# Optimization experiments

Measured on AMD Instinct MI355X. Metric: run time of the kernel, lower is better.

The kernel has to match this reference:

```python
import jax, jax.numpy as jnp
import numpy as np

C = 256
NUM_HEADS = 8
GROUPS = C // 8
EPS = 1e-5


def conv1x1(x, w, b=None):
    # x: (B,C,H,W), w: (O,C)
    y = jnp.einsum('bchw,oc->bohw', x, w)
    if b is not None:
        y = y + b[None, :, None, None]
    return y


def dwconv3x3_s2(x, w):
    # depthwise 3x3, stride 2, padding 1; w: (C,1,3,3)
    return jax.lax.conv_general_dilated(
        x, w, window_strides=(2, 2), padding=((1, 1), (1, 1)),
        feature_group_count=x.shape[1],
        dimension_numbers=('NCHW', 'OIHW', 'NCHW'))


def group_norm(x, scale, bias, groups=GROUPS, eps=EPS):
    B, Cc, H, W = x.shape
    xg = x.reshape(B, groups, Cc // groups, H, W)
    mu = xg.mean(axis=(2, 3, 4), keepdims=True)
    var = xg.var(axis=(2, 3, 4), keepdims=True)
    xn = (xg - mu) * jax.lax.rsqrt(var + eps)
    return xn.reshape(B, Cc, H, W) * scale[None, :, None, None] + bias[None, :, None, None]


def silu(x):
    return x * jax.nn.sigmoid(x)


def downsample_branch(x, dw, gn1_s, gn1_b, pw, gn2_s, gn2_b):
    y = dwconv3x3_s2(x, dw)
    y = silu(group_norm(y, gn1_s, gn1_b))
    y = conv1x1(y, pw)
    y = silu(group_norm(y, gn2_s, gn2_b))
    return y


def setup_inputs() -> dict:
    key = jax.random.key(0)
    ks = jax.random.split(key, 20)
    s = 1.0 / np.sqrt(C)
    inp = {
        'x': jax.random.normal(ks[0], (32, C, 32, 32), dtype=jnp.float32),
        'wq': jax.random.normal(ks[1], (C, C), dtype=jnp.float32) * s,
        'bq': jnp.zeros((C,), jnp.float32),
        'wk': jax.random.normal(ks[2], (C, C), dtype=jnp.float32) * s,
        'bk': jnp.zeros((C,), jnp.float32),
        'wv': jax.random.normal(ks[3], (C, C), dtype=jnp.float32) * s,
        'bv': jnp.zeros((C,), jnp.float32),
        'k_dw': jax.random.normal(ks[4], (C, 1, 3, 3), dtype=jnp.float32) * (1.0 / 3.0),
        'k_gn1_s': jnp.ones((C,), jnp.float32), 'k_gn1_b': jnp.zeros((C,), jnp.float32),
        'k_pw': jax.random.normal(ks[5], (C, C), dtype=jnp.float32) * s,
        'k_gn2_s': jnp.ones((C,), jnp.float32), 'k_gn2_b': jnp.zeros((C,), jnp.float32),
        'v_dw': jax.random.normal(ks[6], (C, 1, 3, 3), dtype=jnp.float32) * (1.0 / 3.0),
        'v_gn1_s': jnp.ones((C,), jnp.float32), 'v_gn1_b': jnp.zeros((C,), jnp.float32),
        'v_pw': jax.random.normal(ks[7], (C, C), dtype=jnp.float32) * s,
        'v_gn2_s': jnp.ones((C,), jnp.float32), 'v_gn2_b': jnp.zeros((C,), jnp.float32),
    }
    return inp


def reference(x, wq, bq, wk, bk, wv, bv,
              k_dw, k_gn1_s, k_gn1_b, k_pw, k_gn2_s, k_gn2_b,
              v_dw, v_gn1_s, v_gn1_b, v_pw, v_gn2_s, v_gn2_b):
    B, Cc, H, W = x.shape
    nh = NUM_HEADS
    Dh = Cc // nh
    q = conv1x1(x, wq, bq)
    k = conv1x1(x, wk, bk)
    v = conv1x1(x, wv, bv)
    k = downsample_branch(k, k_dw, k_gn1_s, k_gn1_b, k_pw, k_gn2_s, k_gn2_b)
    v = downsample_branch(v, v_dw, v_gn1_s, v_gn1_b, v_pw, v_gn2_s, v_gn2_b)
    # view (B, nh, Dh, N) then transpose to (B, nh, N, Dh)
    qh = q.reshape(B, nh, Dh, -1).transpose(0, 1, 3, 2)
    kh = k.reshape(B, nh, Dh, -1).transpose(0, 1, 3, 2)
    vh = v.reshape(B, nh, Dh, -1).transpose(0, 1, 3, 2)
    scores = jnp.einsum('bhnd,bhmd->bhnm', qh, kh) / jnp.sqrt(jnp.float32(Dh))
    attn = jax.nn.softmax(scores, axis=-1)
    out = jnp.einsum('bhnm,bhmd->bhnd', attn, vh)  # (B,nh,N,Dh)
    out = out.transpose(0, 1, 3, 2).reshape(B, Cc, H, W)
    return out
```

## Files before the change

kernel.cpp:

```cpp
#include <hip/hip_runtime.h>
#include <cstddef>

#define B_  32
#define C_  256
#define N_  1024
#define M_  256
#define NH_ 8
#define DH_ 32

typedef __attribute__((ext_vector_type(4))) float f32x4;
typedef _Float16 half8h __attribute__((ext_vector_type(8)));
typedef _Float16 half4h __attribute__((ext_vector_type(4)));
typedef _Float16 half2h __attribute__((ext_vector_type(2)));

#define GLD16(g, l) __builtin_amdgcn_global_load_lds( \
    (const __attribute__((address_space(1))) unsigned int*)(g), \
    (__attribute__((address_space(3))) unsigned int*)(l), 16, 0, 0)

__global__ __launch_bounds__(256) void prep(
    const float* __restrict__ x,
    const float* __restrict__ w0, const float* __restrict__ w1,
    const float* __restrict__ w2, const float* __restrict__ w3,
    const float* __restrict__ w4,
    _Float16* __restrict__ xt, _Float16* __restrict__ wf5)
{
    const int bx = blockIdx.x;
    const int tid = threadIdx.x;

    if (bx < 2048) {
        __shared__ float tile[64][65];
        const int k0 = (bx & 3) * 64;
        const int n0 = ((bx >> 2) & 15) * 64;
        const int b  = bx >> 6;
        #pragma unroll
        for (int i = 0; i < 4; ++i) {
            const int kl = (tid >> 4) + i * 16;
            float4 v = *(const float4*)&x[((size_t)(b * C_) + k0 + kl) * N_ + n0 + (tid & 15) * 4];
            tile[(tid & 15) * 4 + 0][kl] = v.x;
            tile[(tid & 15) * 4 + 1][kl] = v.y;
            tile[(tid & 15) * 4 + 2][kl] = v.z;
            tile[(tid & 15) * 4 + 3][kl] = v.w;
        }
        __syncthreads();
        #pragma unroll
        for (int i = 0; i < 4; ++i) {
            const int nl = (tid >> 4) + i * 16;
            const int kl = (tid & 15) * 4;
            half4h hv;
            hv[0] = (_Float16)tile[nl][kl + 0];
            hv[1] = (_Float16)tile[nl][kl + 1];
            hv[2] = (_Float16)tile[nl][kl + 2];
            hv[3] = (_Float16)tile[nl][kl + 3];
            *(half4h*)&xt[((size_t)(b * N_) + n0 + nl) * C_ + k0 + kl] = hv;
        }
    } else {
        const int wb = bx - 2048;
        const int which = wb >> 4;
        const int off0  = (wb & 15) * 4096;
        const float* src = which == 0 ? w0 : which == 1 ? w1 : which == 2 ? w2
                          : which == 3 ? w3 : w4;
        _Float16* dst = wf5 + (size_t)which * 65536 + off0;
        #pragma unroll
        for (int j = 0; j < 16; ++j)
            dst[tid + j * 256] = (_Float16)src[off0 + tid + j * 256];
    }
}

__global__ __launch_bounds__(256) void qkv_gemm(
    const _Float16* __restrict__ wf5, const _Float16* __restrict__ XT,
    const float* __restrict__ bq, const float* __restrict__ bk,
    const float* __restrict__ bv,
    _Float16* __restrict__ yq, _Float16* __restrict__ yk,
    _Float16* __restrict__ yv)
{
    __shared__ _Float16 Ah[128][32];
    __shared__ _Float16 Bh[128][32];

    const int z = blockIdx.z;
    const int which = z >> 5;
    const int b = z & 31;
    const _Float16* Wf = wf5 + (size_t)which * 65536;
    const float* bias = which == 0 ? bq : which == 1 ? bk : bv;
    _Float16* Y = which == 0 ? yq : which == 1 ? yk : yv;

    const int row0 = blockIdx.x * 128;
    const int n0   = blockIdx.y * 128;
    const int tid  = threadIdx.x;
    const int lane = tid & 63, w = tid >> 6;
    const int wm = (w >> 1) * 64, wn = (w & 1) * 64;
    const int l16 = lane & 15, lq = lane >> 4;

    const _Float16* XTb = XT + ((size_t)(b * N_) + n0) * C_;

    const int sr = lane >> 2;
    const int sc = (lane & 3) * 8;
    const _Float16* Ag0 = Wf  + (size_t)(row0 + w * 32 + sr) * C_ + sc;
    const _Float16* Ag1 = Ag0 + (size_t)16 * C_;
    const _Float16* Bg0 = XTb + (size_t)(w * 32 + sr) * C_ + sc;
    const _Float16* Bg1 = Bg0 + (size_t)16 * C_;
    _Float16* ldsA0 = &Ah[w * 32][0];
    _Float16* ldsA1 = &Ah[w * 32 + 16][0];
    _Float16* ldsB0 = &Bh[w * 32][0];
    _Float16* ldsB1 = &Bh[w * 32 + 16][0];

    f32x4 acc[4][4];
    #pragma unroll
    for (int i = 0; i < 4; ++i)
        #pragma unroll
        for (int j = 0; j < 4; ++j)
            #pragma unroll
            for (int r = 0; r < 4; ++r) acc[i][j][r] = 0.f;

    for (int k0 = 0; k0 < C_; k0 += 32) {
        __syncthreads();
        GLD16(Ag0 + k0, ldsA0);
        GLD16(Ag1 + k0, ldsA1);
        GLD16(Bg0 + k0, ldsB0);
        GLD16(Bg1 + k0, ldsB1);
        __syncthreads();

        half8h af[4], bf[4];
        #pragma unroll
        for (int t = 0; t < 4; ++t) {
            af[t] = *(const half8h*)&Ah[wm + t * 16 + l16][lq * 8];
            bf[t] = *(const half8h*)&Bh[wn + t * 16 + l16][lq * 8];
        }
        #pragma unroll
        for (int mt = 0; mt < 4; ++mt)
            #pragma unroll
            for (int nt = 0; nt < 4; ++nt)
                acc[mt][nt] = __builtin_amdgcn_mfma_f32_16x16x32_f16(af[mt], bf[nt], acc[mt][nt], 0, 0, 0);
    }

    #pragma unroll
    for (int mt = 0; mt < 4; ++mt) {
        #pragma unroll
        for (int r = 0; r < 4; ++r) {
            const int row = row0 + wm + mt * 16 + lq * 4 + r;
            const float bv_ = bias[row];
            #pragma unroll
            for (int nt = 0; nt < 4; ++nt)
                Y[((size_t)(b * C_) + row) * N_ + n0 + wn + nt * 16 + l16] =
                    (_Float16)(acc[mt][nt][r] + bv_);
        }
    }
}

__global__ __launch_bounds__(256) void dw_gn(
    const _Float16* __restrict__ kin, const _Float16* __restrict__ vin,
    const float* __restrict__ kdw, const float* __restrict__ vdw,
    const float* __restrict__ kg1s, const float* __restrict__ kg1b,
    const float* __restrict__ vg1s, const float* __restrict__ vg1b,
    _Float16* __restrict__ kdT, _Float16* __restrict__ vdT)
{
    __shared__ _Float16 Xs[8192];
    __shared__ float red[8];
    const int bx = blockIdx.x;
    const int branch = bx >> 10;
    const int b = (bx >> 5) & 31;
    const int g = bx & 31;
    const _Float16* in = branch ? vin : kin;
    const float* dw = branch ? vdw : kdw;
    const float* gs = branch ? vg1s : kg1s;
    const float* gb = branch ? vg1b : kg1b;
    _Float16* outT = branch ? vdT : kdT;

    const int tid = threadIdx.x;

    {
        const _Float16* src = in + ((size_t)(b * C_) + g * 8) * 1024;
        #pragma unroll
        for (int i = 0; i < 4; ++i)
            *(half8h*)&Xs[tid * 8 + i * 2048] =
                *(const half8h*)&src[tid * 8 + i * 2048];
    }
    __syncthreads();

    const int oy = tid >> 4, ox = tid & 15;
    const int iy0 = oy*2 - 1, ix0 = ox*2 - 1;

    float vals[8];
    float s1 = 0.f, s2 = 0.f;
    #pragma unroll
    for (int cc = 0; cc < 8; ++cc) {
        const int c = g*8 + cc;
        const _Float16* ip = &Xs[cc * 1024];
        const float* wp = dw + c*9;
        float s = 0.f;
        #pragma unroll
        for (int dy = 0; dy < 3; ++dy) {
            const int iy = iy0 + dy;
            if (iy < 0 || iy > 31) continue;
            #pragma unroll
            for (int dx = 0; dx < 3; ++dx) {
                const int ix = ix0 + dx;
                if (ix < 0 || ix > 31) continue;
                s += (float)ip[iy*32 + ix] * wp[dy*3 + dx];
            }
        }
        vals[cc] = s;
        s1 += s; s2 += s*s;
    }
    #pragma unroll
    for (int off = 32; off > 0; off >>= 1) {
        s1 += __shfl_down(s1, off);
        s2 += __shfl_down(s2, off);
    }
    const int lane = tid & 63, wid = tid >> 6;
    if (lane == 0) { red[wid] = s1; red[4 + wid] = s2; }
    __syncthreads();
    s1 = red[0] + red[1] + red[2] + red[3];
    s2 = red[4] + red[5] + red[6] + red[7];
    const float mean = s1 * (1.f/2048.f);
    const float var  = s2 * (1.f/2048.f) - mean*mean;
    const float rstd = rsqrtf(var + 1e-5f);

    half8h o;
    #pragma unroll
    for (int cc = 0; cc < 8; ++cc) {
        const int c = g*8 + cc;
        const float xn = (vals[cc] - mean) * rstd * gs[c] + gb[c];
        o[cc] = (_Float16)(xn / (1.f + __expf(-xn)));
    }
    *(half8h*)&outT[((size_t)(b * M_) + tid) * C_ + g * 8] = o;
}

__global__ __launch_bounds__(256) void pw_gn2(
    const _Float16* __restrict__ wf5,
    const _Float16* __restrict__ kdT, const _Float16* __restrict__ vdT,
    const float* __restrict__ kg2s, const float* __restrict__ kg2b,
    const float* __restrict__ vg2s, const float* __restrict__ vg2b,
    _Float16* __restrict__ k2, _Float16* __restrict__ v2)
{
    __shared__ _Float16 Wlds[32][264];
    __shared__ _Float16 Bs[256][32];
    __shared__ float gmean[4], grstd[4];

    const int ch0 = blockIdx.x * 32;
    const int b   = blockIdx.y;
    const int branch = blockIdx.z;
    const _Float16* Wsrc = wf5 + (size_t)(3 + branch) * 65536;
    const _Float16* inT = branch ? vdT : kdT;
    const float* gs = branch ? vg2s : kg2s;
    const float* gb = branch ? vg2b : kg2b;
    _Float16* outp = branch ? v2 : k2;

    const int tid = threadIdx.x;
    const int lane = tid & 63, w = tid >> 6;
    const int l16 = lane & 15, quad = lane >> 4;

    {
        const int row = tid >> 3;
        const int off = (tid & 7) * 32;
        #pragma unroll
        for (int j = 0; j < 4; ++j)
            *(int4*)&Wlds[row][off + j * 8] =
                *(const int4*)&Wsrc[(size_t)(ch0 + row) * C_ + off + j * 8];
    }

    f32x4 acc[2][4];
    #pragma unroll
    for (int i = 0; i < 2; ++i)
        #pragma unroll
        for (int j = 0; j < 4; ++j)
            #pragma unroll
            for (int r = 0; r < 4; ++r) acc[i][j][r] = 0.f;

    const _Float16* inb = inT + (size_t)(b * M_) * C_;
    const int sr = lane >> 2;
    const int sc = (lane & 3) * 8;
    const _Float16* Bg = inb + (size_t)(w * 64 + sr) * C_ + sc;

    for (int k0 = 0; k0 < C_; k0 += 32) {
        __syncthreads();
        GLD16(Bg + k0,             &Bs[w * 64][0]);
        GLD16(Bg + 16 * C_ + k0,   &Bs[w * 64 + 16][0]);
        GLD16(Bg + 32 * C_ + k0,   &Bs[w * 64 + 32][0]);
        GLD16(Bg + 48 * C_ + k0,   &Bs[w * 64 + 48][0]);
        __syncthreads();

        half8h af[2], bf[4];
        #pragma unroll
        for (int mt = 0; mt < 2; ++mt)
            af[mt] = *(const half8h*)&Wlds[mt * 16 + l16][k0 + quad * 8];
        #pragma unroll
        for (int nt = 0; nt < 4; ++nt)
            bf[nt] = *(const half8h*)&Bs[w * 64 + nt * 16 + l16][quad * 8];
        #pragma unroll
        for (int mt = 0; mt < 2; ++mt)
            #pragma unroll
            for (int nt = 0; nt < 4; ++nt)
                acc[mt][nt] = __builtin_amdgcn_mfma_f32_16x16x32_f16(af[mt], bf[nt], acc[mt][nt], 0, 0, 0);
    }

    __syncthreads();
    _Float16 (*Rs)[264] = Wlds;
    #pragma unroll
    for (int mt = 0; mt < 2; ++mt)
        #pragma unroll
        for (int nt = 0; nt < 4; ++nt)
            #pragma unroll
            for (int r = 0; r < 4; ++r)
                Rs[mt * 16 + quad * 4 + r][w * 64 + nt * 16 + l16] = (_Float16)acc[mt][nt][r];
    __syncthreads();

    {
        float s1 = 0.f, s2 = 0.f;
        #pragma unroll
        for (int r = 0; r < 8; ++r)
            #pragma unroll
            for (int j = 0; j < 4; ++j) {
                const float vv = (float)Rs[w * 8 + r][lane * 4 + j];
                s1 += vv; s2 += vv * vv;
            }
        #pragma unroll
        for (int off = 32; off > 0; off >>= 1) {
            s1 += __shfl_xor(s1, off);
            s2 += __shfl_xor(s2, off);
        }
        if (lane == 0) {
            const float mean = s1 * (1.f / 2048.f);
            const float var  = s2 * (1.f / 2048.f) - mean * mean;
            gmean[w] = mean;
            grstd[w] = rsqrtf(var + 1e-5f);
        }
    }
    __syncthreads();

    #pragma unroll
    for (int cc = 0; cc < 32; ++cc) {
        const int g = cc >> 3;
        const float xn = ((float)Rs[cc][tid] - gmean[g]) * grstd[g] * gs[ch0 + cc] + gb[ch0 + cc];
        const float y  = xn / (1.f + __expf(-xn));
        outp[((size_t)(b * C_) + ch0 + cc) * M_ + tid] = (_Float16)y;
    }
}

__global__ __launch_bounds__(512) void attention_mfma(
    const _Float16* __restrict__ q, const _Float16* __restrict__ k,
    const _Float16* __restrict__ v, float* __restrict__ out)
{
    __shared__ _Float16 Kl[256][40];
    __shared__ _Float16 VT[32][264];

    const int bh = blockIdx.y;
    const int b = bh >> 3, h = bh & 7;
    const int n0 = blockIdx.x * 256;
    const int tid = threadIdx.x;
    const int lane = tid & 63, w = tid >> 6;
    const int l16 = lane & 15, quad = lane >> 4;
    const float qscale = 0.17677669529663687f * 1.4426950408889634f;
    const float SHIFT = 8.0f * 1.4426950408889634f;
    const f32x4 initS = {-SHIFT, -SHIFT, -SHIFT, -SHIFT};

    const size_t kvbase = ((size_t)(b * C_) + h * DH_) * (size_t)M_;

    {
        const int d2 = (tid & 15) * 2;
        const int m0 = (tid >> 4) * 8;
        half8h ka = *(const half8h*)&k[kvbase + (size_t)d2 * M_ + m0];
        half8h kb = *(const half8h*)&k[kvbase + (size_t)(d2 + 1) * M_ + m0];
        #pragma unroll
        for (int j = 0; j < 8; ++j) {
            union { _Float16 h[2]; unsigned u; } pk;
            pk.h[0] = ka[j]; pk.h[1] = kb[j];
            *(unsigned*)&Kl[m0 + j][d2] = pk.u;
        }
        const int vd  = tid & 31;
        const int vm0 = (tid >> 5) * 16;
        #pragma unroll
        for (int i = 0; i < 2; ++i)
            *(half8h*)&VT[vd][vm0 + i * 8] =
                *(const half8h*)&v[kvbase + (size_t)vd * M_ + vm0 + i * 8];
    }

    const int qn = n0 + w * 32 + l16;
    half8h qf[2];
    #pragma unroll
    for (int qt = 0; qt < 2; ++qt)
        #pragma unroll
        for (int j = 0; j < 8; ++j) {
            const float qv = (float)q[((size_t)(b * C_) + h * DH_ + quad * 8 + j) * N_ + qn + qt * 16];
            qf[qt][j] = (_Float16)(qv * qscale);
        }

    __syncthreads();

    f32x4 O[2][2];
    #pragma unroll
    for (int qt = 0; qt < 2; ++qt)
        #pragma unroll
        for (int dt = 0; dt < 2; ++dt)
            #pragma unroll
            for (int r = 0; r < 4; ++r) O[qt][dt][r] = 0.f;
    float lsum[2] = {0.f, 0.f};

    #pragma unroll
    for (int ch = 0; ch < 2; ++ch) {
        f32x4 S[2][8];
        #pragma unroll
        for (int kt = 0; kt < 8; ++kt) {
            half8h kf = *(const half8h*)&Kl[ch * 128 + kt * 16 + l16][quad * 8];
            S[0][kt] = __builtin_amdgcn_mfma_f32_16x16x32_f16(kf, qf[0], initS, 0, 0, 0);
            S[1][kt] = __builtin_amdgcn_mfma_f32_16x16x32_f16(kf, qf[1], initS, 0, 0, 0);
        }
        #pragma unroll
        for (int qt = 0; qt < 2; ++qt)
            #pragma unroll
            for (int kt = 0; kt < 8; ++kt)
                #pragma unroll
                for (int r = 0; r < 4; ++r) {
                    const float p = exp2f(S[qt][kt][r]);
                    S[qt][kt][r] = p;
                    lsum[qt] += p;
                }
        #pragma unroll
        for (int kt = 0; kt < 8; ++kt) {
            half4h vf[2];
            #pragma unroll
            for (int dt = 0; dt < 2; ++dt)
                vf[dt] = *(const half4h*)&VT[dt * 16 + l16][ch * 128 + kt * 16 + quad * 4];
            #pragma unroll
            for (int qt = 0; qt < 2; ++qt) {
                half2h p01 = __builtin_bit_cast(half2h,
                    __builtin_amdgcn_cvt_pkrtz(S[qt][kt][0], S[qt][kt][1]));
                half2h p23 = __builtin_bit_cast(half2h,
                    __builtin_amdgcn_cvt_pkrtz(S[qt][kt][2], S[qt][kt][3]));
                half4h pf = __builtin_shufflevector(p01, p23, 0, 1, 2, 3);
                #pragma unroll
                for (int dt = 0; dt < 2; ++dt)
                    O[qt][dt] = __builtin_amdgcn_mfma_f32_16x16x16f16(vf[dt], pf, O[qt][dt], 0, 0, 0);
            }
        }
    }

    #pragma unroll
    for (int qt = 0; qt < 2; ++qt) {
        float ls = lsum[qt];
        ls += __shfl_xor(ls, 16);
        ls += __shfl_xor(ls, 32);
        const float inv = 1.f / ls;
        #pragma unroll
        for (int dt = 0; dt < 2; ++dt)
            #pragma unroll
            for (int r = 0; r < 4; ++r) {
                const int drow = h * DH_ + dt * 16 + quad * 4 + r;
                out[((size_t)(b * C_) + drow) * N_ + qn + qt * 16] = O[qt][dt][r] * inv;
            }
    }
}

extern "C" void kernel_launch(void* const* d_in, const int* in_sizes, int n_in,
                              void* d_out, int out_size, void* d_ws, size_t ws_size,
                              hipStream_t stream)
{
    const float* x    = (const float*)d_in[0];
    const float* wq   = (const float*)d_in[1];
    const float* bq   = (const float*)d_in[2];
    const float* wk   = (const float*)d_in[3];
    const float* bk   = (const float*)d_in[4];
    const float* wv   = (const float*)d_in[5];
    const float* bv   = (const float*)d_in[6];
    const float* kdw  = (const float*)d_in[7];
    const float* kg1s = (const float*)d_in[8];
    const float* kg1b = (const float*)d_in[9];
    const float* kpw  = (const float*)d_in[10];
    const float* kg2s = (const float*)d_in[11];
    const float* kg2b = (const float*)d_in[12];
    const float* vdw  = (const float*)d_in[13];
    const float* vg1s = (const float*)d_in[14];
    const float* vg1b = (const float*)d_in[15];
    const float* vpw  = (const float*)d_in[16];
    const float* vg2s = (const float*)d_in[17];
    const float* vg2b = (const float*)d_in[18];
    float* out = (float*)d_out;

    const size_t HCN = (size_t)B_ * C_ * N_;
    const size_t HCM = (size_t)B_ * C_ * M_;
    _Float16* qh  = (_Float16*)d_ws;
    _Float16* k0h = qh  + HCN;
    _Float16* v0h = k0h + HCN;
    _Float16* XT  = v0h + HCN;
    _Float16* Wf5 = XT  + HCN;
    _Float16* kdT = Wf5 + 5 * 65536;
    _Float16* vdT = kdT + HCM;
    _Float16* k2  = vdT + HCM;
    _Float16* v2  = k2  + HCM;

    dim3 blk(256);

    prep<<<dim3(2128), blk, 0, stream>>>(x, wq, wk, wv, kpw, vpw, XT, Wf5);
    qkv_gemm<<<dim3(2, 8, 96), blk, 0, stream>>>(Wf5, XT, bq, bk, bv, qh, k0h, v0h);
    dw_gn<<<dim3(2048), blk, 0, stream>>>(k0h, v0h, kdw, vdw,
                                          kg1s, kg1b, vg1s, vg1b, kdT, vdT);
    pw_gn2<<<dim3(8, 32, 2), blk, 0, stream>>>(Wf5, kdT, vdT,
                                               kg2s, kg2b, vg2s, vg2b, k2, v2);
    attention_mfma<<<dim3(4, B_ * NH_), dim3(512), 0, stream>>>(qh, k2, v2, out);
}
```

Baseline: 193.7 us.

## Double-buffer LDS loads in GEMMs and shrink attention score chunks

The QKV GEMM and the pointwise GN2 GEMM now use two LDS buffers. The next K-slice is prefetched via global_load_lds while the current slice feeds MFMA, which drops one barrier per iteration. The attention kernel processes keys in four chunks of 64 instead of two of 128 and converts exp results to packed fp16 right away. This is meant to cut register pressure and interleave exp with MFMA. It doubles LDS use in both GEMMs, which may reduce occupancy.

Measured after the change: 201.4 us. 4.0% more time.

```diff
diff --git a/kernel.cpp b/kernel.cpp
--- a/kernel.cpp
+++ b/kernel.cpp
@@ -73,8 +73,8 @@
     _Float16* __restrict__ yq, _Float16* __restrict__ yk,
     _Float16* __restrict__ yv)
 {
-    __shared__ _Float16 Ah[128][32];
-    __shared__ _Float16 Bh[128][32];
+    __shared__ _Float16 Ah[2][128][32];
+    __shared__ _Float16 Bh[2][128][32];
 
     const int z = blockIdx.z;
     const int which = z >> 5;
@@ -98,10 +98,6 @@
     const _Float16* Ag1 = Ag0 + (size_t)16 * C_;
     const _Float16* Bg0 = XTb + (size_t)(w * 32 + sr) * C_ + sc;
     const _Float16* Bg1 = Bg0 + (size_t)16 * C_;
-    _Float16* ldsA0 = &Ah[w * 32][0];
-    _Float16* ldsA1 = &Ah[w * 32 + 16][0];
-    _Float16* ldsB0 = &Bh[w * 32][0];
-    _Float16* ldsB1 = &Bh[w * 32 + 16][0];
 
     f32x4 acc[4][4];
     #pragma unroll
@@ -111,25 +107,35 @@
             #pragma unroll
             for (int r = 0; r < 4; ++r) acc[i][j][r] = 0.f;
 
-    for (int k0 = 0; k0 < C_; k0 += 32) {
-        __syncthreads();
-        GLD16(Ag0 + k0, ldsA0);
-        GLD16(Ag1 + k0, ldsA1);
-        GLD16(Bg0 + k0, ldsB0);
-        GLD16(Bg1 + k0, ldsB1);
-        __syncthreads();
-
+    GLD16(Ag0, &Ah[0][w * 32][0]);
+    GLD16(Ag1, &Ah[0][w * 32 + 16][0]);
+    GLD16(Bg0, &Bh[0][w * 32][0]);
+    GLD16(Bg1, &Bh[0][w * 32 + 16][0]);
+    __syncthreads();
+
+    #pragma unroll
+    for (int t = 0; t < 8; ++t) {
+        const int cur = t & 1;
+        if (t < 7) {
+            const int kn = (t + 1) * 32;
+            const int nxt = cur ^ 1;
+            GLD16(Ag0 + kn, &Ah[nxt][w * 32][0]);
+            GLD16(Ag1 + kn, &Ah[nxt][w * 32 + 16][0]);
+            GLD16(Bg0 + kn, &Bh[nxt][w * 32][0]);
+            GLD16(Bg1 + kn, &Bh[nxt][w * 32 + 16][0]);
+        }
         half8h af[4], bf[4];
         #pragma unroll
-        for (int t = 0; t < 4; ++t) {
-            af[t] = *(const half8h*)&Ah[wm + t * 16 + l16][lq * 8];
-            bf[t] = *(const half8h*)&Bh[wn + t * 16 + l16][lq * 8];
+        for (int t4 = 0; t4 < 4; ++t4) {
+            af[t4] = *(const half8h*)&Ah[cur][wm + t4 * 16 + l16][lq * 8];
+            bf[t4] = *(const half8h*)&Bh[cur][wn + t4 * 16 + l16][lq * 8];
         }
         #pragma unroll
         for (int mt = 0; mt < 4; ++mt)
             #pragma unroll
             for (int nt = 0; nt < 4; ++nt)
                 acc[mt][nt] = __builtin_amdgcn_mfma_f32_16x16x32_f16(af[mt], bf[nt], acc[mt][nt], 0, 0, 0);
+        if (t < 7) __syncthreads();
     }
 
     #pragma unroll
@@ -233,7 +239,7 @@
     _Float16* __restrict__ k2, _Float16* __restrict__ v2)
 {
     __shared__ _Float16 Wlds[32][264];
-    __shared__ _Float16 Bs[256][32];
+    __shared__ _Float16 Bs[2][256][32];
     __shared__ float gmean[4], grstd[4];
 
     const int ch0 = blockIdx.x * 32;
@@ -249,48 +255,58 @@
     const int lane = tid & 63, w = tid >> 6;
     const int l16 = lane & 15, quad = lane >> 4;
 
-    {
-        const int row = tid >> 3;
-        const int off = (tid & 7) * 32;
-        #pragma unroll
-        for (int j = 0; j < 4; ++j)
-            *(int4*)&Wlds[row][off + j * 8] =
-                *(const int4*)&Wsrc[(size_t)(ch0 + row) * C_ + off + j * 8];
-    }
-
-    f32x4 acc[2][4];
-    #pragma unroll
-    for (int i = 0; i < 2; ++i)
-        #pragma unroll
-        for (int j = 0; j < 4; ++j)
-            #pragma unroll
-            for (int r = 0; r < 4; ++r) acc[i][j][r] = 0.f;
-
     const _Float16* inb = inT + (size_t)(b * M_) * C_;
     const int sr = lane >> 2;
     const int sc = (lane & 3) * 8;
     const _Float16* Bg = inb + (size_t)(w * 64 + sr) * C_ + sc;
 
-    for (int k0 = 0; k0 < C_; k0 += 32) {
-        __syncthreads();
-        GLD16(Bg + k0,             &Bs[w * 64][0]);
-        GLD16(Bg + 16 * C_ + k0,   &Bs[w * 64 + 16][0]);
-        GLD16(Bg + 32 * C_ + k0,   &Bs[w * 64 + 32][0]);
-        GLD16(Bg + 48 * C_ + k0,   &Bs[w * 64 + 48][0]);
-        __syncthreads();
-
+    {
+        const int row = tid >> 3;
+        const int off = (tid & 7) * 32;
+        #pragma unroll
+        for (int j = 0; j < 4; ++j)
+            *(int4*)&Wlds[row][off + j * 8] =
+                *(const int4*)&Wsrc[(size_t)(ch0 + row) * C_ + off + j * 8];
+    }
+    GLD16(Bg,           &Bs[0][w * 64][0]);
+    GLD16(Bg + 16 * C_, &Bs[0][w * 64 + 16][0]);
+    GLD16(Bg + 32 * C_, &Bs[0][w * 64 + 32][0]);
+    GLD16(Bg + 48 * C_, &Bs[0][w * 64 + 48][0]);
+
+    f32x4 acc[2][4];
+    #pragma unroll
+    for (int i = 0; i < 2; ++i)
+        #pragma unroll
+        for (int j = 0; j < 4; ++j)
+            #pragma unroll
+            for (int r = 0; r < 4; ++r) acc[i][j][r] = 0.f;
+
+    __syncthreads();
+
+    #pragma unroll
+    for (int t = 0; t < 8; ++t) {
+        const int cur = t & 1;
+        if (t < 7) {
+            const int kn = (t + 1) * 32;
+            const int nxt = cur ^ 1;
+            GLD16(Bg + kn,           &Bs[nxt][w * 64][0]);
+            GLD16(Bg + 16 * C_ + kn, &Bs[nxt][w * 64 + 16][0]);
+            GLD16(Bg + 32 * C_ + kn, &Bs[nxt][w * 64 + 32][0]);
+            GLD16(Bg + 48 * C_ + kn, &Bs[nxt][w * 64 + 48][0]);
+        }
         half8h af[2], bf[4];
         #pragma unroll
         for (int mt = 0; mt < 2; ++mt)
-            af[mt] = *(const half8h*)&Wlds[mt * 16 + l16][k0 + quad * 8];
+            af[mt] = *(const half8h*)&Wlds[mt * 16 + l16][t * 32 + quad * 8];
         #pragma unroll
         for (int nt = 0; nt < 4; ++nt)
-            bf[nt] = *(const half8h*)&Bs[w * 64 + nt * 16 + l16][quad * 8];
+            bf[nt] = *(const half8h*)&Bs[cur][w * 64 + nt * 16 + l16][quad * 8];
         #pragma unroll
         for (int mt = 0; mt < 2; ++mt)
             #pragma unroll
             for (int nt = 0; nt < 4; ++nt)
                 acc[mt][nt] = __builtin_amdgcn_mfma_f32_16x16x32_f16(af[mt], bf[nt], acc[mt][nt], 0, 0, 0);
+        if (t < 7) __syncthreads();
     }
 
     __syncthreads();
@@ -396,41 +412,38 @@
     float lsum[2] = {0.f, 0.f};
 
     #pragma unroll
-    for (int ch = 0; ch < 2; ++ch) {
-        f32x4 S[2][8];
-        #pragma unroll
-        for (int kt = 0; kt < 8; ++kt) {
-            half8h kf = *(const half8h*)&Kl[ch * 128 + kt * 16 + l16][quad * 8];
-            S[0][kt] = __builtin_amdgcn_mfma_f32_16x16x32_f16(kf, qf[0], initS, 0, 0, 0);
-            S[1][kt] = __builtin_amdgcn_mfma_f32_16x16x32_f16(kf, qf[1], initS, 0, 0, 0);
-        }
-        #pragma unroll
-        for (int qt = 0; qt < 2; ++qt)
-            #pragma unroll
-            for (int kt = 0; kt < 8; ++kt)
-                #pragma unroll
-                for (int r = 0; r < 4; ++r) {
-                    const float p = exp2f(S[qt][kt][r]);
-                    S[qt][kt][r] = p;
-                    lsum[qt] += p;
-                }
-        #pragma unroll
-        for (int kt = 0; kt < 8; ++kt) {
-            half4h vf[2];
-            #pragma unroll
-            for (int dt = 0; dt < 2; ++dt)
-                vf[dt] = *(const half4h*)&VT[dt * 16 + l16][ch * 128 + kt * 16 + quad * 4];
-            #pragma unroll
-            for (int qt = 0; qt < 2; ++qt) {
-                half2h p01 = __builtin_bit_cast(half2h,
-                    __builtin_amdgcn_cvt_pkrtz(S[qt][kt][0], S[qt][kt][1]));
-                half2h p23 = __builtin_bit_cast(half2h,
-                    __builtin_amdgcn_cvt_pkrtz(S[qt][kt][2], S[qt][kt][3]));
-                half4h pf = __builtin_shufflevector(p01, p23, 0, 1, 2, 3);
-                #pragma unroll
-                for (int dt = 0; dt < 2; ++dt)
-                    O[qt][dt] = __builtin_amdgcn_mfma_f32_16x16x16f16(vf[dt], pf, O[qt][dt], 0, 0, 0);
-            }
+    for (int ch = 0; ch < 4; ++ch) {
+        f32x4 S0[4], S1[4];
+        #pragma unroll
+        for (int kt = 0; kt < 4; ++kt) {
+            half8h kf = *(const half8h*)&Kl[ch * 64 + kt * 16 + l16][quad * 8];
+            S0[kt] = __builtin_amdgcn_mfma_f32_16x16x32_f16(kf, qf[0], initS, 0, 0, 0);
+            S1[kt] = __builtin_amdgcn_mfma_f32_16x16x32_f16(kf, qf[1], initS, 0, 0, 0);
+        }
+        half4h pf0[4], pf1[4];
+        #pragma unroll
+        for (int kt = 0; kt < 4; ++kt) {
+            float a0 = exp2f(S0[kt][0]), a1 = exp2f(S0[kt][1]);
+            float a2 = exp2f(S0[kt][2]), a3 = exp2f(S0[kt][3]);
+            lsum[0] += (a0 + a1) + (a2 + a3);
+            half2h u01 = __builtin_bit_cast(half2h, __builtin_amdgcn_cvt_pkrtz(a0, a1));
+            half2h u23 = __builtin_bit_cast(half2h, __builtin_amdgcn_cvt_pkrtz(a2, a3));
+            pf0[kt] = __builtin_shufflevector(u01, u23, 0, 1, 2, 3);
+            float b0 = exp2f(S1[kt][0]), b1 = exp2f(S1[kt][1]);
+            float b2 = exp2f(S1[kt][2]), b3 = exp2f(S1[kt][3]);
+            lsum[1] += (b0 + b1) + (b2 + b3);
+            half2h v01 = __builtin_bit_cast(half2h, __builtin_amdgcn_cvt_pkrtz(b0, b1));
+            half2h v23 = __builtin_bit_cast(half2h, __builtin_amdgcn_cvt_pkrtz(b2, b3));
+            pf1[kt] = __builtin_shufflevector(v01, v23, 0, 1, 2, 3);
+        }
+        #pragma unroll
+        for (int kt = 0; kt < 4; ++kt) {
+            half4h vf0 = *(const half4h*)&VT[l16][ch * 64 + kt * 16 + quad * 4];
+            half4h vf1 = *(const half4h*)&VT[16 + l16][ch * 64 + kt * 16 + quad * 4];
+            O[0][0] = __builtin_amdgcn_mfma_f32_16x16x16f16(vf0, pf0[kt], O[0][0], 0, 0, 0);
+            O[0][1] = __builtin_amdgcn_mfma_f32_16x16x16f16(vf1, pf0[kt], O[0][1], 0, 0, 0);
+            O[1][0] = __builtin_amdgcn_mfma_f32_16x16x16f16(vf0, pf1[kt], O[1][0], 0, 0, 0);
+            O[1][1] = __builtin_amdgcn_mfma_f32_16x16x16f16(vf1, pf1[kt], O[1][1], 0, 0, 0);
         }
     }
 
```

## Store Q head-transposed with prescale in GEMM epilogue; add MFMA priority hints

Applied to the files above, without the earlier changes.

The QKV projection epilogue now writes Q in a (B, heads, N, Dh) layout, with bias and the softmax scale times log2e already applied. This lets the attention kernel load each Q fragment with a single 16-byte vector load instead of 16 strided scalar loads plus conversions. The attention loop also wraps its MFMA sections in s_setprio raises so waves issuing matrix ops get scheduling priority over waves doing exp work. The GEMM's Q stores become 8-byte scattered writes with a stride of Dh, which may coalesce worse than the old row-contiguous stores.

New measurement: 199.4 us. +2.9%, slower.

```diff
diff --git a/kernel.cpp b/kernel.cpp
--- a/kernel.cpp
+++ b/kernel.cpp
@@ -132,16 +132,38 @@
                 acc[mt][nt] = __builtin_amdgcn_mfma_f32_16x16x32_f16(af[mt], bf[nt], acc[mt][nt], 0, 0, 0);
     }
 
-    #pragma unroll
-    for (int mt = 0; mt < 4; ++mt) {
-        #pragma unroll
-        for (int r = 0; r < 4; ++r) {
-            const int row = row0 + wm + mt * 16 + lq * 4 + r;
-            const float bv_ = bias[row];
-            #pragma unroll
-            for (int nt = 0; nt < 4; ++nt)
-                Y[((size_t)(b * C_) + row) * N_ + n0 + wn + nt * 16 + l16] =
-                    (_Float16)(acc[mt][nt][r] + bv_);
+    if (which == 0) {
+        const float qs = 0.17677669529663687f * 1.4426950408889634f;
+        #pragma unroll
+        for (int mt = 0; mt < 4; ++mt) {
+            const int row = row0 + wm + mt * 16 + lq * 4;
+            const float4 bv4 = *(const float4*)&bias[row];
+            const int h  = row >> 5;
+            const int d0 = row & 31;
+            _Float16* yh = Y + ((size_t)(b * NH_) + h) * N_ * DH_ + d0;
+            #pragma unroll
+            for (int nt = 0; nt < 4; ++nt) {
+                const int n = n0 + wn + nt * 16 + l16;
+                half4h hv;
+                hv[0] = (_Float16)((acc[mt][nt][0] + bv4.x) * qs);
+                hv[1] = (_Float16)((acc[mt][nt][1] + bv4.y) * qs);
+                hv[2] = (_Float16)((acc[mt][nt][2] + bv4.z) * qs);
+                hv[3] = (_Float16)((acc[mt][nt][3] + bv4.w) * qs);
+                *(half4h*)&yh[(size_t)n * DH_] = hv;
+            }
+        }
+    } else {
+        #pragma unroll
+        for (int mt = 0; mt < 4; ++mt) {
+            #pragma unroll
+            for (int r = 0; r < 4; ++r) {
+                const int row = row0 + wm + mt * 16 + lq * 4 + r;
+                const float bv_ = bias[row];
+                #pragma unroll
+                for (int nt = 0; nt < 4; ++nt)
+                    Y[((size_t)(b * C_) + row) * N_ + n0 + wn + nt * 16 + l16] =
+                        (_Float16)(acc[mt][nt][r] + bv_);
+            }
         }
     }
 }
@@ -337,7 +359,7 @@
 }
 
 __global__ __launch_bounds__(512) void attention_mfma(
-    const _Float16* __restrict__ q, const _Float16* __restrict__ k,
+    const _Float16* __restrict__ qT, const _Float16* __restrict__ k,
     const _Float16* __restrict__ v, float* __restrict__ out)
 {
     __shared__ _Float16 Kl[256][40];
@@ -349,7 +371,6 @@
     const int tid = threadIdx.x;
     const int lane = tid & 63, w = tid >> 6;
     const int l16 = lane & 15, quad = lane >> 4;
-    const float qscale = 0.17677669529663687f * 1.4426950408889634f;
     const float SHIFT = 8.0f * 1.4426950408889634f;
     const f32x4 initS = {-SHIFT, -SHIFT, -SHIFT, -SHIFT};
 
@@ -375,14 +396,10 @@
     }
 
     const int qn = n0 + w * 32 + l16;
+    const _Float16* qbase = qT + (((size_t)(b * NH_) + h) * N_ + qn) * DH_ + quad * 8;
     half8h qf[2];
-    #pragma unroll
-    for (int qt = 0; qt < 2; ++qt)
-        #pragma unroll
-        for (int j = 0; j < 8; ++j) {
-            const float qv = (float)q[((size_t)(b * C_) + h * DH_ + quad * 8 + j) * N_ + qn + qt * 16];
-            qf[qt][j] = (_Float16)(qv * qscale);
-        }
+    qf[0] = *(const half8h*)&qbase[0];
+    qf[1] = *(const half8h*)&qbase[16 * DH_];
 
     __syncthreads();
 
@@ -398,12 +415,14 @@
     #pragma unroll
     for (int ch = 0; ch < 2; ++ch) {
         f32x4 S[2][8];
+        __builtin_amdgcn_s_setprio(1);
         #pragma unroll
         for (int kt = 0; kt < 8; ++kt) {
             half8h kf = *(const half8h*)&Kl[ch * 128 + kt * 16 + l16][quad * 8];
             S[0][kt] = __builtin_amdgcn_mfma_f32_16x16x32_f16(kf, qf[0], initS, 0, 0, 0);
             S[1][kt] = __builtin_amdgcn_mfma_f32_16x16x32_f16(kf, qf[1], initS, 0, 0, 0);
         }
+        __builtin_amdgcn_s_setprio(0);
         #pragma unroll
         for (int qt = 0; qt < 2; ++qt)
             #pragma unroll
@@ -414,6 +433,7 @@
                     S[qt][kt][r] = p;
                     lsum[qt] += p;
                 }
+        __builtin_amdgcn_s_setprio(1);
         #pragma unroll
         for (int kt = 0; kt < 8; ++kt) {
             half4h vf[2];
@@ -432,6 +452,7 @@
                     O[qt][dt] = __builtin_amdgcn_mfma_f32_16x16x16f16(vf[dt], pf, O[qt][dt], 0, 0, 0);
             }
         }
+        __builtin_amdgcn_s_setprio(0);
     }
 
     #pragma unroll
```
